# Kernel optimization log

Hardware: AMD Instinct MI355X
Metric: run time of the kernel (lower is better)

Reference implementation:

```python
import jax, jax.numpy as jnp
import numpy as np

NEG_INF = -1e30

def _rotary_tables(n_pos, d_k):
    # angular_freq = (1/10000)**linspace(0,1,d_k//4), padded with d_k//4 zeros -> d_k//2 freqs
    freqs = (1.0 / 10000.0) ** jnp.linspace(0.0, 1.0, d_k // 4, dtype=jnp.float32)
    freqs = jnp.concatenate([freqs, jnp.zeros(d_k // 4, dtype=jnp.float32)])  # [d_k//2]
    t = jnp.arange(n_pos, dtype=jnp.float32)
    theta = t[:, None] * freqs[None, :]  # [n_pos, d_k//2]
    return jnp.cos(theta), jnp.sin(theta)

def _apply_rotary(x_bhtd, cos, sin):
    # Faithful to torch source: cos/sin are indexed/broadcast along dim -3,
    # which for [B,H,T,D] input is the HEAD axis (original code's quirk).
    c = cos[None, :, None, :]  # [1,H,1,D/2]
    s = sin[None, :, None, :]
    x1, x2 = jnp.split(x_bhtd, 2, axis=-1)
    y1 = x1 * c + x2 * s
    y2 = -x1 * s + x2 * c
    return jnp.concatenate([y1, y2], axis=-1)

def setup_inputs() -> dict:
    key = jax.random.key(0)
    k1, k2, k3 = jax.random.split(key, 3)
    B, S, D = 4, 2048, 2048
    x = jax.random.normal(k1, (B, S, D), dtype=jnp.float32)
    Wqkv = jax.random.normal(k2, (D, 3 * D), dtype=jnp.float32) * (D ** -0.5)
    Wo = jax.random.normal(k3, (D, D), dtype=jnp.float32) * (D ** -0.5)
    return {"x": x, "Wqkv": Wqkv, "Wo": Wo, "n_heads": 16}

def reference(x, Wqkv, Wo, n_heads):
    B, S, D = x.shape
    H = int(n_heads)
    d_k = D // H
    qkv = (x @ Wqkv).reshape(B, S, 3, H, d_k)
    qkv = jnp.transpose(qkv, (2, 0, 3, 1, 4))  # [3,B,H,S,dk]
    Q, K, V = qkv[0], qkv[1], qkv[2]
    cos, sin = _rotary_tables(H, d_k)  # indexed by head axis, per original code
    Q = _apply_rotary(Q, cos, sin)
    K = _apply_rotary(K, cos, sin)
    scores = jnp.einsum('bhqd,bhkd->bhqk', Q, K) / jnp.sqrt(jnp.float32(d_k))
    causal = jnp.tril(jnp.ones((S, S), dtype=bool))
    scores = jnp.where(causal[None, None, :, :], scores, NEG_INF)
    attn = jax.nn.softmax(scores, axis=-1)
    out = jnp.einsum('bhqk,bhkd->bhqd', attn, V)  # [B,H,S,dk]
    out = jnp.transpose(out, (0, 2, 1, 3)).reshape(B, S, D)
    return out @ Wo
```

## Files before the change

### kernel.cpp

```cpp
#include <hip/hip_runtime.h>

typedef __attribute__((ext_vector_type(8))) short short8;
typedef __attribute__((ext_vector_type(4))) short short4v;
typedef __attribute__((ext_vector_type(4))) float f32x4;

__device__ inline short f2bf(float f) {
    union { float f; unsigned u; } v; v.f = f;
    unsigned r = v.u + 0x7fffu + ((v.u >> 16) & 1u);
    return (short)(r >> 16);
}

__device__ __forceinline__ void gload16(const short* g, short* l) {
    __builtin_amdgcn_global_load_lds(
        (const __attribute__((address_space(1))) unsigned int*)g,
        (__attribute__((address_space(3))) unsigned int*)l, 16, 0, 0);
}

__global__ __launch_bounds__(256) void cvt_f32_to_bf16(const float* __restrict__ in,
                                                       short* __restrict__ out, int n4) {
    int i = blockIdx.x * 256 + threadIdx.x;
    if (i >= n4) return;
    float4 v = ((const float4*)in)[i];
    short4v o;
    o[0] = f2bf(v.x); o[1] = f2bf(v.y); o[2] = f2bf(v.z); o[3] = f2bf(v.w);
    ((short4v*)out)[i] = o;
}

__global__ __launch_bounds__(256) void transpose_to_bf16(const float* __restrict__ in,
                                                         short* __restrict__ out,
                                                         int R, int C) {
    __shared__ short tile[64][66];
    int r0 = blockIdx.x * 64, c0 = blockIdx.y * 64;
    int tid = threadIdx.x;
#pragma unroll
    for (int i = 0; i < 16; i++) {
        int idx = i * 256 + tid;
        int r = idx >> 6, c = idx & 63;
        tile[r][c] = f2bf(in[(size_t)(r0 + r) * C + (c0 + c)]);
    }
    __syncthreads();
#pragma unroll
    for (int i = 0; i < 16; i++) {
        int idx = i * 256 + tid;
        int c = idx >> 6, r = idx & 63;
        out[(size_t)(c0 + c) * R + (r0 + r)] = tile[r][c];
    }
}

template <int EPI>
__global__ __launch_bounds__(512) void gemm256(const short* __restrict__ A,
                                               const short* __restrict__ Bt,
                                               int M, int N, int K,
                                               short* __restrict__ O0, short* __restrict__ O1,
                                               short* __restrict__ O2, float* __restrict__ OF,
                                               float qscale) {
    __shared__ short As[4][256 * 32];
    __shared__ short Bs[4][256 * 32];
    int tid = threadIdx.x, lane = tid & 63, wid = tid >> 6;
    int wr = wid >> 2, wc = wid & 3;
    int mtn = M >> 8;
    int band = mtn >> 3;
    int bid = blockIdx.x;
    int xcd = bid & 7, kk = bid >> 3;
    int nt = kk / band, gmr = kk % band;
    int mt = xcd * band + gmr;
    int row0 = mt << 8, col0 = nt << 8;
    int t15 = lane & 15, t4 = lane >> 4;
    int NT = K >> 5;

    f32x4 acc[8][4];
#pragma unroll
    for (int m = 0; m < 8; m++)
#pragma unroll
        for (int n = 0; n < 4; n++) acc[m][n] = (f32x4){0.f, 0.f, 0.f, 0.f};

    int sg = (lane & 3) ^ ((lane >> 3) & 3);
    int srw = lane >> 2;
    int ce = t4 ^ ((t15 >> 1) & 3);

    auto stageA = [&](int t) {
        if (t >= NT) return;
        int kb = t << 5;
        short* dst = &As[t & 3][0];
#pragma unroll
        for (int i = 0; i < 2; i++) {
            int seg = wid * 2 + i;
            int row = seg * 16 + srw;
            gload16(A + (size_t)(row0 + row) * K + kb + sg * 8, dst + seg * 512);
        }
    };
    auto stageB = [&](int t) {
        if (t >= NT) return;
        int kb = t << 5;
        short* dst = &Bs[t & 3][0];
#pragma unroll
        for (int i = 0; i < 2; i++) {
            int seg = wid * 2 + i;
            int row = seg * 16 + srw;
            gload16(Bt + (size_t)(col0 + row) * K + kb + sg * 8, dst + seg * 512);
        }
    };

    stageA(0); stageB(0);
    stageA(1); stageB(1);
    stageA(2); stageB(2);
    asm volatile("s_waitcnt vmcnt(8)" ::: "memory");
    asm volatile("s_barrier" ::: "memory");

    for (int t = 0; t < NT; t++) {
        int bufi = t & 3;
        short8 af[8], bf[4];
#pragma unroll
        for (int m = 0; m < 8; m++) {
            int row = wr * 128 + m * 16 + t15;
            af[m] = *(short8*)(&As[bufi][row * 32 + ce * 8]);
        }
#pragma unroll
        for (int n = 0; n < 4; n++) {
            int row = wc * 64 + n * 16 + t15;
            bf[n] = *(short8*)(&Bs[bufi][row * 32 + ce * 8]);
        }
        stageA(t + 3); stageB(t + 3);

        __builtin_amdgcn_s_setprio(1);
#pragma unroll
        for (int m = 0; m < 8; m++)
#pragma unroll
            for (int n = 0; n < 4; n++)
                acc[m][n] = __builtin_amdgcn_mfma_f32_16x16x32_bf16(af[m], bf[n], acc[m][n], 0, 0, 0);
        __builtin_amdgcn_s_setprio(0);

        if (t + 3 < NT)       asm volatile("s_waitcnt vmcnt(8)" ::: "memory");
        else if (t + 3 == NT) asm volatile("s_waitcnt vmcnt(4)" ::: "memory");
        else                  asm volatile("s_waitcnt vmcnt(0)" ::: "memory");
        asm volatile("s_barrier" ::: "memory");
    }

#pragma unroll
    for (int m = 0; m < 8; m++) {
#pragma unroll
        for (int n = 0; n < 4; n++) {
#pragma unroll
            for (int r = 0; r < 4; r++) {
                float v = acc[m][n][r];
                int gm2 = row0 + wr * 128 + m * 16 + t4 * 4 + r;
                int gn = col0 + wc * 64 + n * 16 + t15;
                if (EPI == 0) {
                    int part = gn >> 11, within = gn & 2047;
                    int h = within >> 7, dk = within & 127;
                    int bb = gm2 >> 11, s = gm2 & 2047;
                    int z = bb * 16 + h;
                    if (part == 0) O0[((size_t)z * 2048 + s) * 128 + dk] = f2bf(v * qscale);
                    else if (part == 1) O1[((size_t)z * 2048 + s) * 128 + dk] = f2bf(v);
                    else O2[((size_t)z * 128 + dk) * 2048 + s] = f2bf(v);
                } else {
                    OF[(size_t)gm2 * N + gn] = v;
                }
            }
        }
    }
}

__global__ __launch_bounds__(512, 4) void attn_fwd(const short* __restrict__ Q,
                                                   const short* __restrict__ Kb,
                                                   const short* __restrict__ Vt,
                                                   short* __restrict__ O) {
    __shared__ short Kls[2][64 * 128];
    __shared__ short Vls[128 * 64];
    __shared__ __align__(16) short Pls[8][16 * 64];
    int tid = threadIdx.x, lane = tid & 63, wid = tid >> 6;
    int bx = blockIdx.x, z = blockIdx.y;
    int pr = bx >> 1, hh = bx & 1;
    int qpan = (wid < 4) ? pr : (15 - pr);
    int t15 = lane & 15, t4 = lane >> 4;
    const short* Qh = Q + (size_t)z * 2048 * 128;
    const short* Kh = Kb + (size_t)z * 2048 * 128;
    const short* Vh = Vt + (size_t)z * 128 * 2048;
    int q0w = qpan * 128 + hh * 64 + (wid & 3) * 16;

    short8 qf[4];
    {
        const short* qrow = Qh + (size_t)(q0w + t15) * 128;
#pragma unroll
        for (int s = 0; s < 4; s++) qf[s] = *(const short8*)(qrow + s * 32 + t4 * 8);
    }

    f32x4 o[8];
#pragma unroll
    for (int st = 0; st < 8; st++) o[st] = (f32x4){0.f, 0.f, 0.f, 0.f};
    float m_s = -1e30f, l_s = 0.f;

    auto stageK = [&](int t, int buf) {
#pragma unroll
        for (int i = 0; i < 2; i++) {
            int seg = wid * 2 + i;
            int row = seg * 4 + t4;
            int kl = (lane & 15) ^ (row & 7);
            gload16(Kh + (size_t)(t * 64 + row) * 128 + kl * 8, &Kls[buf][seg * 512]);
        }
    };
    auto stageV = [&](int t) {
#pragma unroll
        for (int i = 0; i < 2; i++) {
            int seg = wid * 2 + i;
            int row = seg * 8 + (lane >> 3);
            int kl = (lane & 7) ^ (row & 7);
            gload16(Vh + (size_t)row * 2048 + t * 64 + kl * 8, &Vls[seg * 512]);
        }
    };

    int nt = 2 * (15 - pr) + 2;
    stageK(0, 0);
    __syncthreads();

    for (int t = 0; t < nt; t++) {
        int buf = t & 1;
        stageV(t);
        if (t + 1 < nt) stageK(t + 1, buf ^ 1);
        bool active = (t * 64 <= q0w + 15);

        if (active) {
            f32x4 sc[4];
#pragma unroll
            for (int c = 0; c < 4; c++) {
                sc[c] = (f32x4){0.f, 0.f, 0.f, 0.f};
#pragma unroll
                for (int s = 0; s < 4; s++) {
                    int row = c * 16 + t15;
                    int ck = (s * 4 + t4) ^ (row & 7);
                    short8 kf = *(short8*)(&Kls[buf][row * 128 + ck * 8]);
                    sc[c] = __builtin_amdgcn_mfma_f32_16x16x32_bf16(kf, qf[s], sc[c], 0, 0, 0);
                }
            }

            if (t * 64 + 63 > q0w) {
                int qq = q0w + t15;
#pragma unroll
                for (int c = 0; c < 4; c++)
#pragma unroll
                    for (int r = 0; r < 4; r++) {
                        int kv = t * 64 + c * 16 + t4 * 4 + r;
                        if (kv > qq) sc[c][r] = -1e30f;
                    }
            }

            float tm = fmaxf(fmaxf(fmaxf(sc[0][0], sc[0][1]), fmaxf(sc[0][2], sc[0][3])),
                             fmaxf(fmaxf(sc[1][0], sc[1][1]), fmaxf(sc[1][2], sc[1][3])));
            tm = fmaxf(tm, fmaxf(fmaxf(fmaxf(sc[2][0], sc[2][1]), fmaxf(sc[2][2], sc[2][3])),
                                 fmaxf(fmaxf(sc[3][0], sc[3][1]), fmaxf(sc[3][2], sc[3][3]))));
            bool need = (tm > m_s + 8.f);
            if (__any(need)) {
                tm = fmaxf(tm, __shfl_xor(tm, 16));
                tm = fmaxf(tm, __shfl_xor(tm, 32));
                float mn = fmaxf(m_s, tm);
                float scf = exp2f(m_s - mn);
                m_s = mn;
                l_s *= scf;
                float sr0 = __shfl(scf, t4 * 4 + 0);
                float sr1 = __shfl(scf, t4 * 4 + 1);
                float sr2 = __shfl(scf, t4 * 4 + 2);
                float sr3 = __shfl(scf, t4 * 4 + 3);
#pragma unroll
                for (int st = 0; st < 8; st++) {
                    o[st][0] *= sr0; o[st][1] *= sr1;
                    o[st][2] *= sr2; o[st][3] *= sr3;
                }
            }
            int t15l = t15 & 7;
#pragma unroll
            for (int c = 0; c < 4; c++) {
                float p0 = exp2f(sc[c][0] - m_s);
                float p1 = exp2f(sc[c][1] - m_s);
                float p2 = exp2f(sc[c][2] - m_s);
                float p3 = exp2f(sc[c][3] - m_s);
                l_s += (p0 + p1) + (p2 + p3);
                unsigned u0, u1;
                asm("v_cvt_pk_bf16_f32 %0, %1, %2" : "=v"(u0) : "v"(p0), "v"(p1));
                asm("v_cvt_pk_bf16_f32 %0, %1, %2" : "=v"(u1) : "v"(p2), "v"(p3));
                int ch = (c * 2 + (t4 >> 1)) ^ t15l;
                uint2 uu; uu.x = u0; uu.y = u1;
                *(uint2*)((char*)&Pls[wid][0] + t15 * 128 + ch * 16 + (t4 & 1) * 8) = uu;
            }
        }

        __syncthreads();

        if (active) {
            short8 pa[2];
#pragma unroll
            for (int s2 = 0; s2 < 2; s2++) {
                int ch2 = (s2 * 4 + t4) ^ (t15 & 7);
                pa[s2] = *(short8*)((char*)&Pls[wid][0] + t15 * 128 + ch2 * 16);
            }
#pragma unroll
            for (int st = 0; st < 8; st++) {
#pragma unroll
                for (int s2 = 0; s2 < 2; s2++) {
                    int row = st * 16 + t15;
                    int ck = (s2 * 4 + t4) ^ (row & 7);
                    short8 vf = *(short8*)(&Vls[row * 64 + ck * 8]);
                    o[st] = __builtin_amdgcn_mfma_f32_16x16x32_bf16(pa[s2], vf, o[st], 0, 0, 0);
                }
            }
        }

        __syncthreads();
    }

    l_s += __shfl_xor(l_s, 16);
    l_s += __shfl_xor(l_s, 32);
    float lr0 = __shfl(l_s, t4 * 4 + 0);
    float lr1 = __shfl(l_s, t4 * 4 + 1);
    float lr2 = __shfl(l_s, t4 * 4 + 2);
    float lr3 = __shfl(l_s, t4 * 4 + 3);
    float lr[4] = {lr0, lr1, lr2, lr3};

    int b = z >> 4, h = z & 15;
#pragma unroll
    for (int st = 0; st < 8; st++)
#pragma unroll
        for (int r = 0; r < 4; r++) {
            int s = q0w + t4 * 4 + r;
            float val = o[st][r] / lr[r];
            O[((size_t)b * 2048 + s) * 2048 + h * 128 + st * 16 + t15] = f2bf(val);
        }
}

extern "C" void kernel_launch(void* const* d_in, const int* in_sizes, int n_in,
                              void* d_out, int out_size, void* d_ws, size_t ws_size,
                              hipStream_t stream) {
    const float* x = (const float*)d_in[0];
    const float* Wqkv = (const float*)d_in[1];
    const float* Wo = (const float*)d_in[2];

    const int B = 4, S = 2048, D = 2048, DK = 128;
    const int M = B * S;
    const int N1 = 3 * D;
    (void)in_sizes; (void)n_in; (void)out_size; (void)ws_size;

    char* ws = (char*)d_ws;
    size_t off = 0;
    short* x_bf = (short*)(ws + off);   off += (size_t)M * D * 2;
    short* wqkv_t = (short*)(ws + off); off += (size_t)N1 * D * 2;
    short* wo_t = (short*)(ws + off);   off += (size_t)D * D * 2;
    short* Qb = (short*)(ws + off);     off += (size_t)64 * S * DK * 2;
    short* Kb = (short*)(ws + off);     off += (size_t)64 * S * DK * 2;
    short* Vt = (short*)(ws + off);     off += (size_t)64 * S * DK * 2;
    short* Ob = (short*)(ws + off);     off += (size_t)M * D * 2;

    cvt_f32_to_bf16<<<(M * D / 4 + 255) / 256, 256, 0, stream>>>(x, x_bf, M * D / 4);
    transpose_to_bf16<<<dim3(D / 64, N1 / 64, 1), 256, 0, stream>>>(Wqkv, wqkv_t, D, N1);
    transpose_to_bf16<<<dim3(D / 64, D / 64, 1), 256, 0, stream>>>(Wo, wo_t, D, D);
    gemm256<0><<<(M / 256) * (N1 / 256), 512, 0, stream>>>(
        x_bf, wqkv_t, M, N1, D, Qb, Kb, Vt, nullptr, 0.12751743553366927f);
    attn_fwd<<<dim3(16, 64), 512, 0, stream>>>(Qb, Kb, Vt, Ob);
    gemm256<1><<<(M / 256) * (D / 256), 512, 0, stream>>>(
        Ob, wo_t, M, D, D, nullptr, nullptr, nullptr, (float*)d_out, 1.0f);
}
```

Baseline: 436.2 us.

## Use 128x128 GEMM for output projection and remap attention query panels

Adds a new 128x128-tile bf16 MFMA GEMM with a triple-buffered LDS pipeline and XCD-aware block mapping, and uses it for the output projection instead of the 256-tile GEMM. The aim is more workgroups, and so better CU fill, for the 8192x2048 output. Separately, the attention kernel no longer pairs a short and a long causal panel inside one block. Each block now handles one full 128-row query panel with 8 waves, launched longest first, which changes load balance across blocks.

After: 500.5 us. +14.7%, slower.

```diff
diff --git a/kernel.cpp b/kernel.cpp
--- a/kernel.cpp
+++ b/kernel.cpp
@@ -161,6 +161,90 @@
     }
 }
 
+__global__ __launch_bounds__(256) void gemm128(const short* __restrict__ A,
+                                               const short* __restrict__ Bt,
+                                               int M, int N, int K,
+                                               float* __restrict__ OF) {
+    __shared__ short As[3][128 * 32];
+    __shared__ short Bs[3][128 * 32];
+    int tid = threadIdx.x, lane = tid & 63, wid = tid >> 6;
+    int wr = wid >> 1, wc = wid & 1;
+    int bid = blockIdx.x;
+    int xcd = bid & 7;
+    int k = bid >> 3;
+    int nt = k >> 3;
+    int gm = k & 7;
+    int mt = (xcd << 3) + gm;
+    int row0 = mt << 7, col0 = nt << 7;
+    int t15 = lane & 15, t4 = lane >> 4;
+    int sg = (lane & 3) ^ ((lane >> 3) & 3);
+    int srw = lane >> 2;
+    int ce = t4 ^ ((t15 >> 1) & 3);
+    int NT = K >> 5;
+
+    f32x4 acc[4][4];
+#pragma unroll
+    for (int m = 0; m < 4; m++)
+#pragma unroll
+        for (int n = 0; n < 4; n++) acc[m][n] = (f32x4){0.f, 0.f, 0.f, 0.f};
+
+    auto stage = [&](int t) {
+        if (t >= NT) return;
+        int kb = t << 5;
+        int b = t % 3;
+#pragma unroll
+        for (int i = 0; i < 2; i++) {
+            int seg = wid * 2 + i;
+            int row = seg * 16 + srw;
+            gload16(A + (size_t)(row0 + row) * K + kb + sg * 8, &As[b][seg * 512]);
+            gload16(Bt + (size_t)(col0 + row) * K + kb + sg * 8, &Bs[b][seg * 512]);
+        }
+    };
+
+    stage(0); stage(1);
+    asm volatile("s_waitcnt vmcnt(4)" ::: "memory");
+    asm volatile("s_barrier" ::: "memory");
+
+    for (int t = 0; t < NT; t++) {
+        int b = t % 3;
+        short8 af[4], bf[4];
+#pragma unroll
+        for (int m = 0; m < 4; m++) {
+            int row = wr * 64 + m * 16 + t15;
+            af[m] = *(short8*)(&As[b][row * 32 + ce * 8]);
+        }
+#pragma unroll
+        for (int n = 0; n < 4; n++) {
+            int row = wc * 64 + n * 16 + t15;
+            bf[n] = *(short8*)(&Bs[b][row * 32 + ce * 8]);
+        }
+        stage(t + 2);
+
+        __builtin_amdgcn_s_setprio(1);
+#pragma unroll
+        for (int m = 0; m < 4; m++)
+#pragma unroll
+            for (int n = 0; n < 4; n++)
+                acc[m][n] = __builtin_amdgcn_mfma_f32_16x16x32_bf16(af[m], bf[n], acc[m][n], 0, 0, 0);
+        __builtin_amdgcn_s_setprio(0);
+
+        if (t + 2 < NT) asm volatile("s_waitcnt vmcnt(4)" ::: "memory");
+        else            asm volatile("s_waitcnt vmcnt(0)" ::: "memory");
+        asm volatile("s_barrier" ::: "memory");
+    }
+
+#pragma unroll
+    for (int m = 0; m < 4; m++)
+#pragma unroll
+        for (int n = 0; n < 4; n++)
+#pragma unroll
+            for (int r = 0; r < 4; r++) {
+                int gm2 = row0 + wr * 64 + m * 16 + t4 * 4 + r;
+                int gn = col0 + wc * 64 + n * 16 + t15;
+                OF[(size_t)gm2 * N + gn] = acc[m][n][r];
+            }
+}
+
 __global__ __launch_bounds__(512, 4) void attn_fwd(const short* __restrict__ Q,
                                                    const short* __restrict__ Kb,
                                                    const short* __restrict__ Vt,
@@ -170,13 +254,12 @@
     __shared__ __align__(16) short Pls[8][16 * 64];
     int tid = threadIdx.x, lane = tid & 63, wid = tid >> 6;
     int bx = blockIdx.x, z = blockIdx.y;
-    int pr = bx >> 1, hh = bx & 1;
-    int qpan = (wid < 4) ? pr : (15 - pr);
+    int qpan = 15 - bx;
     int t15 = lane & 15, t4 = lane >> 4;
     const short* Qh = Q + (size_t)z * 2048 * 128;
     const short* Kh = Kb + (size_t)z * 2048 * 128;
     const short* Vh = Vt + (size_t)z * 128 * 2048;
-    int q0w = qpan * 128 + hh * 64 + (wid & 3) * 16;
+    int q0w = qpan * 128 + wid * 16;
 
     short8 qf[4];
     {
@@ -209,7 +292,7 @@
         }
     };
 
-    int nt = 2 * (15 - pr) + 2;
+    int nt = 2 * qpan + 2;
     stageK(0, 0);
     __syncthreads();
 
@@ -354,6 +437,5 @@
     gemm256<0><<<(M / 256) * (N1 / 256), 512, 0, stream>>>(
         x_bf, wqkv_t, M, N1, D, Qb, Kb, Vt, nullptr, 0.12751743553366927f);
     attn_fwd<<<dim3(16, 64), 512, 0, stream>>>(Qb, Kb, Vt, Ob);
-    gemm256<1><<<(M / 256) * (D / 256), 512, 0, stream>>>(
-        Ob, wo_t, M, D, D, nullptr, nullptr, nullptr, (float*)d_out, 1.0f);
-}
+    gemm128<<<(M / 128) * (D / 128), 256, 0, stream>>>(Ob, wo_t, M, D, D, (float*)d_out);
+}
```
